# Performance work log

Measured on AMD Instinct MI355X. Metric: run time of the kernel, lower is better.

The kernel has to match this reference:

```python
import jax, jax.numpy as jnp
import numpy as np

EMB = 256          # embedding_size
P = 2              # scoring_norm
EPS = 1e-6
APPLY_TANH = True
DIST_PER_DIM = True
N_REL = 1024
BATCH = 131072


def setup_inputs() -> dict:
    key = jax.random.key(0)
    k1, k2, k3, k4 = jax.random.split(key, 4)
    head_emb = jax.random.normal(k1, (BATCH, 2 * EMB), dtype=jnp.float32)
    tail_emb = jax.random.normal(k2, (BATCH, 2 * EMB), dtype=jnp.float32)
    relation_id = jax.random.randint(k3, (BATCH,), 0, N_REL, dtype=jnp.int32)
    # relation row = [center_h | center_t | width_h | width_t | size_h | size_t]
    relation_embedding = jax.random.uniform(k4, (N_REL, 4 * EMB + 2), dtype=jnp.float32)
    return {"head_emb": head_emb, "relation_id": relation_id,
            "tail_emb": tail_emb, "relation_embedding": relation_embedding}


def _boxe_score(bumped_ht, center_ht, width_ht, box_size):
    # bumped_ht/center_ht/width_ht: (B, 2, EMB); box_size: (B, 2)
    width = jnp.abs(width_ht)
    # geometric-mean normalization of box widths (softened by EPS)
    gmean = jnp.exp(jnp.mean(jnp.log(jnp.clip(width, EPS, None)), axis=-1, keepdims=True))
    width = width / jnp.clip(gmean, EPS, None)
    width = width * (1.0 + jax.nn.elu(box_size[..., None].astype(width.dtype)))
    if APPLY_TANH:
        width = jnp.tanh(width)
        center_ht = jnp.tanh(center_ht)
        bumped_ht = jnp.tanh(bumped_ht)
    width_p1 = width + 1.0
    center_dist = jnp.abs(bumped_ht - center_ht)
    # kappa = 0.5 * w * (w+1 - 1/(w+1))
    kappa = 0.5 * width * (width_p1 - 1.0 / width_p1)
    in_box = center_dist <= width / 2.0
    if not DIST_PER_DIM:
        in_box = jnp.all(in_box, axis=-1, keepdims=True)
    dist = jnp.where(in_box, center_dist / width_p1, center_dist * width_p1 - kappa)
    # p-norm over embedding dim -> (B, 2); negative sum of head+tail scores
    norm = jnp.power(jnp.sum(jnp.power(jnp.abs(dist), P), axis=-1), 1.0 / P)
    return -jnp.sum(norm, axis=-1)


def reference(head_emb, relation_id, tail_emb, relation_embedding):
    rel = relation_embedding[relation_id]                       # (B, 4*EMB+2)
    B = head_emb.shape[0]
    center_ht = rel[:, : 2 * EMB].reshape(B, 2, EMB)
    width_ht = rel[:, 2 * EMB : 4 * EMB].reshape(B, 2, EMB)
    box_size = rel[:, 4 * EMB :].reshape(B, 2)
    head_pos, head_bump = head_emb[:, :EMB], head_emb[:, EMB:]
    tail_pos, tail_bump = tail_emb[:, :EMB], tail_emb[:, EMB:]
    # bumped heads scored vs head box, bumped tails vs tail box
    bumped_ht = jnp.stack([head_pos + tail_bump, tail_pos + head_bump], axis=1)  # (B,2,EMB)
    return _boxe_score(bumped_ht, center_ht, width_ht, box_size)
```

## Files before the change

kernel.cpp:

```cpp
#include <hip/hip_runtime.h>

constexpr int EMB = 256;
constexpr float FEPS = 1e-6f;
constexpr int RELDIMS = 2 * EMB;
constexpr size_t PRE_FLOATS = 1024u * RELDIMS * 2;
constexpr size_t PRE_BYTES  = PRE_FLOATS * sizeof(float);

__device__ __forceinline__ float ftanh(float x) {
    x = fminf(15.f, fmaxf(-15.f, x));
    float t = __expf(2.f * x);
    return (t - 1.f) * __builtin_amdgcn_rcpf(t + 1.f);
}

__global__ __launch_bounds__(256) void boxe_pre(
    const float* __restrict__ rel, int n_rel, float* __restrict__ pre)
{
    const int r    = (blockIdx.x * blockDim.x + threadIdx.x) >> 6;
    const int lane = threadIdx.x & 63;
    if (r >= n_rel) return;
    const float* __restrict__ rrow = rel + (long)r * (4 * EMB + 2);
    const int d0 = lane * 4;

    float c0[4], c1[4], w0[4], w1[4];
    *(float4*)c0 = *(const float4*)(rrow + d0);
    *(float4*)c1 = *(const float4*)(rrow + EMB + d0);
    *(float4*)w0 = *(const float4*)(rrow + 2 * EMB + d0);
    *(float4*)w1 = *(const float4*)(rrow + 3 * EMB + d0);
    const float bs0 = rrow[4 * EMB + 0];
    const float bs1 = rrow[4 * EMB + 1];

    float wa0[4], wa1[4], ls0 = 0.f, ls1 = 0.f;
#pragma unroll
    for (int j = 0; j < 4; ++j) {
        wa0[j] = fabsf(w0[j]);
        wa1[j] = fabsf(w1[j]);
        ls0 += __logf(fmaxf(wa0[j], FEPS));
        ls1 += __logf(fmaxf(wa1[j], FEPS));
    }
#pragma unroll
    for (int off = 32; off >= 1; off >>= 1) {
        ls0 += __shfl_xor(ls0, off, 64);
        ls1 += __shfl_xor(ls1, off, 64);
    }
    const float g0 = __expf(ls0 * (1.f / (float)EMB));
    const float g1 = __expf(ls1 * (1.f / (float)EMB));
    const float e0 = (bs0 > 0.f) ? bs0 : (__expf(bs0) - 1.f);
    const float e1 = (bs1 > 0.f) ? bs1 : (__expf(bs1) - 1.f);
    const float s0 = (1.f + e0) / fmaxf(g0, FEPS);
    const float s1 = (1.f + e1) / fmaxf(g1, FEPS);

    float* __restrict__ prow = pre + (long)r * (RELDIMS * 2);
    float pa[4], pb[4];
#pragma unroll
    for (int j = 0; j < 4; ++j) {
        float ct  = ftanh(c0[j]);
        float wp1 = ftanh(wa0[j] * s0) + 1.f;
        if (j < 2) { pa[j * 2] = ct; pa[j * 2 + 1] = wp1; }
        else       { pb[(j - 2) * 2] = ct; pb[(j - 2) * 2 + 1] = wp1; }
    }
    *(float4*)(prow + d0 * 2)     = *(float4*)pa;
    *(float4*)(prow + d0 * 2 + 4) = *(float4*)pb;
#pragma unroll
    for (int j = 0; j < 4; ++j) {
        float ct  = ftanh(c1[j]);
        float wp1 = ftanh(wa1[j] * s1) + 1.f;
        if (j < 2) { pa[j * 2] = ct; pa[j * 2 + 1] = wp1; }
        else       { pb[(j - 2) * 2] = ct; pb[(j - 2) * 2 + 1] = wp1; }
    }
    *(float4*)(prow + (EMB + d0) * 2)     = *(float4*)pa;
    *(float4*)(prow + (EMB + d0) * 2 + 4) = *(float4*)pb;
}

__device__ __forceinline__ float d2term(float ct, float wp1, float bm, float& ) {
    return 0.f;
}

__global__ __launch_bounds__(256) void boxe_main(
    const float* __restrict__ head, const int* __restrict__ rid,
    const float* __restrict__ tail, const float* __restrict__ pre,
    float* __restrict__ out, int batch)
{
    const int b    = (int)(((size_t)blockIdx.x * blockDim.x + threadIdx.x) >> 6);
    const int lane = threadIdx.x & 63;
    if (b >= batch) return;

    const int r  = rid[b];
    const int d0 = lane * 4;
    const float* __restrict__ hrow = head + (long)b * RELDIMS;
    const float* __restrict__ trow = tail + (long)b * RELDIMS;
    const float* __restrict__ prow = pre + (long)r * (RELDIMS * 2);

    float hp[4], hb[4], tp[4], tb[4];
    *(float4*)hp = *(const float4*)(hrow + d0);
    *(float4*)hb = *(const float4*)(hrow + EMB + d0);
    *(float4*)tp = *(const float4*)(trow + d0);
    *(float4*)tb = *(const float4*)(trow + EMB + d0);

    float p0[8], p1[8];
    *(float4*)(p0)     = *(const float4*)(prow + d0 * 2);
    *(float4*)(p0 + 4) = *(const float4*)(prow + d0 * 2 + 4);
    *(float4*)(p1)     = *(const float4*)(prow + (EMB + d0) * 2);
    *(float4*)(p1 + 4) = *(const float4*)(prow + (EMB + d0) * 2 + 4);

    float acc0 = 0.f, acc1 = 0.f;
#pragma unroll
    for (int j = 0; j < 4; ++j) {
        {
            float ct  = p0[j * 2], wp1 = p0[j * 2 + 1];
            float w   = wp1 - 1.f;
            float inv = __builtin_amdgcn_rcpf(wp1);
            float bt  = ftanh(hp[j] + tb[j]);
            float cd  = fabsf(bt - ct);
            float kap = 0.5f * w * (wp1 - inv);
            float d   = (cd <= 0.5f * w) ? (cd * inv) : fmaf(cd, wp1, -kap);
            acc0 = fmaf(d, d, acc0);
        }
        {
            float ct  = p1[j * 2], wp1 = p1[j * 2 + 1];
            float w   = wp1 - 1.f;
            float inv = __builtin_amdgcn_rcpf(wp1);
            float bt  = ftanh(tp[j] + hb[j]);
            float cd  = fabsf(bt - ct);
            float kap = 0.5f * w * (wp1 - inv);
            float d   = (cd <= 0.5f * w) ? (cd * inv) : fmaf(cd, wp1, -kap);
            acc1 = fmaf(d, d, acc1);
        }
    }
#pragma unroll
    for (int off = 32; off >= 1; off >>= 1) {
        acc0 += __shfl_xor(acc0, off, 64);
        acc1 += __shfl_xor(acc1, off, 64);
    }
    if (lane == 0) out[b] = -(sqrtf(acc0) + sqrtf(acc1));
}

__device__ __forceinline__ float dist2_term(float wabs, float scale, float c, float bm) {
    float w   = ftanh(wabs * scale);
    float ctv = ftanh(c);
    float bt  = ftanh(bm);
    float cd  = fabsf(bt - ctv);
    float wp1 = w + 1.f;
    float inv = __builtin_amdgcn_rcpf(wp1);
    float kappa = 0.5f * w * (wp1 - inv);
    float dist = (cd <= 0.5f * w) ? (cd * inv) : fmaf(cd, wp1, -kappa);
    return dist * dist;
}

__global__ __launch_bounds__(256) void boxe_fused(
    const float* __restrict__ head, const int* __restrict__ rid,
    const float* __restrict__ tail, const float* __restrict__ rel,
    float* __restrict__ out, int batch)
{
    const int b    = (int)(((size_t)blockIdx.x * blockDim.x + threadIdx.x) >> 6);
    const int lane = threadIdx.x & 63;
    if (b >= batch) return;
    const long r = rid[b];
    const float* __restrict__ rrow = rel  + r * (long)(4 * EMB + 2);
    const float* __restrict__ hrow = head + (long)b * RELDIMS;
    const float* __restrict__ trow = tail + (long)b * RELDIMS;
    const int d0 = lane * 4;
    float hp[4], hb[4], tp[4], tb[4], c0[4], c1[4], w0[4], w1[4];
    *(float4*)hp = *(const float4*)(hrow + d0);
    *(float4*)hb = *(const float4*)(hrow + EMB + d0);
    *(float4*)tp = *(const float4*)(trow + d0);
    *(float4*)tb = *(const float4*)(trow + EMB + d0);
    *(float4*)c0 = *(const float4*)(rrow + d0);
    *(float4*)c1 = *(const float4*)(rrow + EMB + d0);
    *(float4*)w0 = *(const float4*)(rrow + 2 * EMB + d0);
    *(float4*)w1 = *(const float4*)(rrow + 3 * EMB + d0);
    const float bs0 = rrow[4 * EMB + 0];
    const float bs1 = rrow[4 * EMB + 1];
    float wa0[4], wa1[4], ls0 = 0.f, ls1 = 0.f;
#pragma unroll
    for (int j = 0; j < 4; ++j) {
        wa0[j] = fabsf(w0[j]); wa1[j] = fabsf(w1[j]);
        ls0 += __logf(fmaxf(wa0[j], FEPS)); ls1 += __logf(fmaxf(wa1[j], FEPS));
    }
#pragma unroll
    for (int off = 32; off >= 1; off >>= 1) {
        ls0 += __shfl_xor(ls0, off, 64); ls1 += __shfl_xor(ls1, off, 64);
    }
    const float g0 = __expf(ls0 * (1.f / 256.f)), g1 = __expf(ls1 * (1.f / 256.f));
    const float e0 = (bs0 > 0.f) ? bs0 : (__expf(bs0) - 1.f);
    const float e1 = (bs1 > 0.f) ? bs1 : (__expf(bs1) - 1.f);
    const float s0 = (1.f + e0) / fmaxf(g0, FEPS);
    const float s1 = (1.f + e1) / fmaxf(g1, FEPS);
    float acc0 = 0.f, acc1 = 0.f;
#pragma unroll
    for (int j = 0; j < 4; ++j) {
        acc0 += dist2_term(wa0[j], s0, c0[j], hp[j] + tb[j]);
        acc1 += dist2_term(wa1[j], s1, c1[j], tp[j] + hb[j]);
    }
#pragma unroll
    for (int off = 32; off >= 1; off >>= 1) {
        acc0 += __shfl_xor(acc0, off, 64); acc1 += __shfl_xor(acc1, off, 64);
    }
    if (lane == 0) out[b] = -(sqrtf(acc0) + sqrtf(acc1));
}

extern "C" void kernel_launch(void* const* d_in, const int* in_sizes, int n_in,
                              void* d_out, int out_size, void* d_ws, size_t ws_size,
                              hipStream_t stream) {
    const float* head = (const float*)d_in[0];
    const int*   rid  = (const int*)d_in[1];
    const float* tail = (const float*)d_in[2];
    const float* rel  = (const float*)d_in[3];
    float* out = (float*)d_out;

    const int batch = out_size;
    const int n_rel = in_sizes[3] / (4 * EMB + 2);
    const int blocks = (batch + 3) / 4;

    const size_t need = (size_t)n_rel * RELDIMS * 2 * sizeof(float);
    if (ws_size >= need && n_rel <= 1024) {
        float* pre = (float*)d_ws;
        boxe_pre<<<(n_rel + 3) / 4, 256, 0, stream>>>(rel, n_rel, pre);
        boxe_main<<<blocks, 256, 0, stream>>>(head, rid, tail, pre, out, batch);
    } else {
        boxe_fused<<<blocks, 256, 0, stream>>>(head, rid, tail, rel, out, batch);
    }
}
```

Measured before the change: 126.5 us.

## Pack precomputed relation table to fp16 and process 8 rows per wave with prefetch

New measurement: 114.2 us. -9.7%, faster.

```diff
diff --git a/kernel.cpp b/kernel.cpp
--- a/kernel.cpp
+++ b/kernel.cpp
@@ -1,10 +1,11 @@
 #include <hip/hip_runtime.h>
+#include <hip/hip_fp16.h>
 
 constexpr int EMB = 256;
+constexpr int RELDIMS = 512;
 constexpr float FEPS = 1e-6f;
-constexpr int RELDIMS = 2 * EMB;
-constexpr size_t PRE_FLOATS = 1024u * RELDIMS * 2;
-constexpr size_t PRE_BYTES  = PRE_FLOATS * sizeof(float);
+constexpr int ROWS = 8;
+constexpr int WPB  = 4;
 
 __device__ __forceinline__ float ftanh(float x) {
     x = fminf(15.f, fmaxf(-15.f, x));
@@ -13,7 +14,7 @@
 }
 
 __global__ __launch_bounds__(256) void boxe_pre(
-    const float* __restrict__ rel, int n_rel, float* __restrict__ pre)
+    const float* __restrict__ rel, int n_rel, unsigned int* __restrict__ pre)
 {
     const int r    = (blockIdx.x * blockDim.x + threadIdx.x) >> 6;
     const int lane = threadIdx.x & 63;
@@ -32,8 +33,7 @@
     float wa0[4], wa1[4], ls0 = 0.f, ls1 = 0.f;
 #pragma unroll
     for (int j = 0; j < 4; ++j) {
-        wa0[j] = fabsf(w0[j]);
-        wa1[j] = fabsf(w1[j]);
+        wa0[j] = fabsf(w0[j]); wa1[j] = fabsf(w1[j]);
         ls0 += __logf(fmaxf(wa0[j], FEPS));
         ls1 += __logf(fmaxf(wa1[j], FEPS));
     }
@@ -49,89 +49,98 @@
     const float s0 = (1.f + e0) / fmaxf(g0, FEPS);
     const float s1 = (1.f + e1) / fmaxf(g1, FEPS);
 
-    float* __restrict__ prow = pre + (long)r * (RELDIMS * 2);
-    float pa[4], pb[4];
-#pragma unroll
-    for (int j = 0; j < 4; ++j) {
-        float ct  = ftanh(c0[j]);
-        float wp1 = ftanh(wa0[j] * s0) + 1.f;
-        if (j < 2) { pa[j * 2] = ct; pa[j * 2 + 1] = wp1; }
-        else       { pb[(j - 2) * 2] = ct; pb[(j - 2) * 2 + 1] = wp1; }
-    }
-    *(float4*)(prow + d0 * 2)     = *(float4*)pa;
-    *(float4*)(prow + d0 * 2 + 4) = *(float4*)pb;
-#pragma unroll
-    for (int j = 0; j < 4; ++j) {
-        float ct  = ftanh(c1[j]);
-        float wp1 = ftanh(wa1[j] * s1) + 1.f;
-        if (j < 2) { pa[j * 2] = ct; pa[j * 2 + 1] = wp1; }
-        else       { pb[(j - 2) * 2] = ct; pb[(j - 2) * 2 + 1] = wp1; }
-    }
-    *(float4*)(prow + (EMB + d0) * 2)     = *(float4*)pa;
-    *(float4*)(prow + (EMB + d0) * 2 + 4) = *(float4*)pb;
-}
-
-__device__ __forceinline__ float d2term(float ct, float wp1, float bm, float& ) {
-    return 0.f;
-}
-
-__global__ __launch_bounds__(256) void boxe_main(
+    unsigned int* __restrict__ prow = pre + (long)r * RELDIMS;
+    unsigned int pk[4];
+#pragma unroll
+    for (int j = 0; j < 4; ++j) {
+        __half2 h2 = __floats2half2_rn(ftanh(c0[j]), ftanh(wa0[j] * s0) + 1.f);
+        pk[j] = *(unsigned int*)&h2;
+    }
+    *(uint4*)(prow + d0) = make_uint4(pk[0], pk[1], pk[2], pk[3]);
+#pragma unroll
+    for (int j = 0; j < 4; ++j) {
+        __half2 h2 = __floats2half2_rn(ftanh(c1[j]), ftanh(wa1[j] * s1) + 1.f);
+        pk[j] = *(unsigned int*)&h2;
+    }
+    *(uint4*)(prow + EMB + d0) = make_uint4(pk[0], pk[1], pk[2], pk[3]);
+}
+
+__global__ __launch_bounds__(256, 4) void boxe_main(
     const float* __restrict__ head, const int* __restrict__ rid,
-    const float* __restrict__ tail, const float* __restrict__ pre,
-    float* __restrict__ out, int batch)
+    const float* __restrict__ tail, const unsigned int* __restrict__ pre,
+    float* __restrict__ out)
 {
-    const int b    = (int)(((size_t)blockIdx.x * blockDim.x + threadIdx.x) >> 6);
+    const int wave = blockIdx.x * WPB + (threadIdx.x >> 6);
     const int lane = threadIdx.x & 63;
-    if (b >= batch) return;
-
-    const int r  = rid[b];
-    const int d0 = lane * 4;
-    const float* __restrict__ hrow = head + (long)b * RELDIMS;
-    const float* __restrict__ trow = tail + (long)b * RELDIMS;
-    const float* __restrict__ prow = pre + (long)r * (RELDIMS * 2);
-
-    float hp[4], hb[4], tp[4], tb[4];
-    *(float4*)hp = *(const float4*)(hrow + d0);
-    *(float4*)hb = *(const float4*)(hrow + EMB + d0);
-    *(float4*)tp = *(const float4*)(trow + d0);
-    *(float4*)tb = *(const float4*)(trow + EMB + d0);
-
-    float p0[8], p1[8];
-    *(float4*)(p0)     = *(const float4*)(prow + d0 * 2);
-    *(float4*)(p0 + 4) = *(const float4*)(prow + d0 * 2 + 4);
-    *(float4*)(p1)     = *(const float4*)(prow + (EMB + d0) * 2);
-    *(float4*)(p1 + 4) = *(const float4*)(prow + (EMB + d0) * 2 + 4);
-
-    float acc0 = 0.f, acc1 = 0.f;
-#pragma unroll
-    for (int j = 0; j < 4; ++j) {
-        {
-            float ct  = p0[j * 2], wp1 = p0[j * 2 + 1];
+    const int b0   = wave * ROWS;
+
+    const int fidx = lane * 8;
+    const int tidx = (lane ^ 32) * 8;
+
+    int ridv[ROWS];
+    {
+        int4 ra = *(const int4*)(rid + b0);
+        int4 rb = *(const int4*)(rid + b0 + 4);
+        ridv[0] = ra.x; ridv[1] = ra.y; ridv[2] = ra.z; ridv[3] = ra.w;
+        ridv[4] = rb.x; ridv[5] = rb.y; ridv[6] = rb.z; ridv[7] = rb.w;
+    }
+
+    float4 hbuf[2][2], tbuf[2][2];
+    uint4  pbuf[2][2];
+
+    {
+        const float* hrow = head + (size_t)b0 * RELDIMS;
+        const float* trow = tail + (size_t)b0 * RELDIMS;
+        const unsigned int* prow = pre + (size_t)ridv[0] * RELDIMS;
+        hbuf[0][0] = *(const float4*)(hrow + fidx);
+        hbuf[0][1] = *(const float4*)(hrow + fidx + 4);
+        tbuf[0][0] = *(const float4*)(trow + tidx);
+        tbuf[0][1] = *(const float4*)(trow + tidx + 4);
+        pbuf[0][0] = *(const uint4*)(prow + fidx);
+        pbuf[0][1] = *(const uint4*)(prow + fidx + 4);
+    }
+
+#pragma unroll
+    for (int i = 0; i < ROWS; ++i) {
+        const int cur = i & 1, nxt = cur ^ 1;
+        if (i + 1 < ROWS) {
+            const int bn = b0 + i + 1;
+            const float* hrow = head + (size_t)bn * RELDIMS;
+            const float* trow = tail + (size_t)bn * RELDIMS;
+            const unsigned int* prow = pre + (size_t)ridv[i + 1] * RELDIMS;
+            hbuf[nxt][0] = *(const float4*)(hrow + fidx);
+            hbuf[nxt][1] = *(const float4*)(hrow + fidx + 4);
+            tbuf[nxt][0] = *(const float4*)(trow + tidx);
+            tbuf[nxt][1] = *(const float4*)(trow + tidx + 4);
+            pbuf[nxt][0] = *(const uint4*)(prow + fidx);
+            pbuf[nxt][1] = *(const uint4*)(prow + fidx + 4);
+        }
+
+        float h[8], t[8];
+        unsigned int pw[8];
+        *(float4*)(h)     = hbuf[cur][0]; *(float4*)(h + 4) = hbuf[cur][1];
+        *(float4*)(t)     = tbuf[cur][0]; *(float4*)(t + 4) = tbuf[cur][1];
+        *(uint4*)(pw)     = pbuf[cur][0]; *(uint4*)(pw + 4) = pbuf[cur][1];
+
+        float acc = 0.f;
+#pragma unroll
+        for (int j = 0; j < 8; ++j) {
+            float2 cw = __half22float2(*(__half2*)&pw[j]);
+            float ct = cw.x, wp1 = cw.y;
+            float bt  = ftanh(h[j] + t[j]);
+            float cd  = fabsf(bt - ct);
             float w   = wp1 - 1.f;
             float inv = __builtin_amdgcn_rcpf(wp1);
-            float bt  = ftanh(hp[j] + tb[j]);
-            float cd  = fabsf(bt - ct);
             float kap = 0.5f * w * (wp1 - inv);
             float d   = (cd <= 0.5f * w) ? (cd * inv) : fmaf(cd, wp1, -kap);
-            acc0 = fmaf(d, d, acc0);
+            acc = fmaf(d, d, acc);
         }
-        {
-            float ct  = p1[j * 2], wp1 = p1[j * 2 + 1];
-            float w   = wp1 - 1.f;
-            float inv = __builtin_amdgcn_rcpf(wp1);
-            float bt  = ftanh(tp[j] + hb[j]);
-            float cd  = fabsf(bt - ct);
-            float kap = 0.5f * w * (wp1 - inv);
-            float d   = (cd <= 0.5f * w) ? (cd * inv) : fmaf(cd, wp1, -kap);
-            acc1 = fmaf(d, d, acc1);
-        }
-    }
-#pragma unroll
-    for (int off = 32; off >= 1; off >>= 1) {
-        acc0 += __shfl_xor(acc0, off, 64);
-        acc1 += __shfl_xor(acc1, off, 64);
-    }
-    if (lane == 0) out[b] = -(sqrtf(acc0) + sqrtf(acc1));
+#pragma unroll
+        for (int off = 16; off >= 1; off >>= 1)
+            acc += __shfl_xor(acc, off, 64);
+        float other = __shfl_xor(acc, 32, 64);
+        if (lane == 0) out[b0 + i] = -(sqrtf(acc) + sqrtf(other));
+    }
 }
 
 __device__ __forceinline__ float dist2_term(float wabs, float scale, float c, float bm) {
@@ -209,14 +218,15 @@
 
     const int batch = out_size;
     const int n_rel = in_sizes[3] / (4 * EMB + 2);
-    const int blocks = (batch + 3) / 4;
-
-    const size_t need = (size_t)n_rel * RELDIMS * 2 * sizeof(float);
-    if (ws_size >= need && n_rel <= 1024) {
-        float* pre = (float*)d_ws;
+    const size_t need = (size_t)n_rel * RELDIMS * sizeof(unsigned int);
+
+    if (ws_size >= need && batch % (WPB * ROWS) == 0) {
+        unsigned int* pre = (unsigned int*)d_ws;
         boxe_pre<<<(n_rel + 3) / 4, 256, 0, stream>>>(rel, n_rel, pre);
-        boxe_main<<<blocks, 256, 0, stream>>>(head, rid, tail, pre, out, batch);
+        const int blocks = batch / (WPB * ROWS);
+        boxe_main<<<blocks, 256, 0, stream>>>(head, rid, tail, pre, out);
     } else {
+        const int blocks = (batch + 3) / 4;
         boxe_fused<<<blocks, 256, 0, stream>>>(head, rid, tail, rel, out, batch);
     }
 }
```
